# Kernel tuning notes

Hardware: AMD Instinct MI355X
Metric: run time of the kernel (lower is better)

## Reference

```python
import jax, jax.numpy as jnp
import numpy as np


def _flip_sequences(inputs, lengths):
    # Keeps padding at the end while reversing the valid prefix (per example).
    T = inputs.shape[1]
    def one(x, L):
        return jnp.flip(jnp.roll(x, T - L, axis=0), axis=0)
    return jax.vmap(one)(inputs, lengths)


def _gru_direction(xy, mask, Wi, Wh, bi, bhn):
    # xy: [B,T,D], mask: [B,T] (True = padding -> carry old state)
    B = xy.shape[0]
    H = bhn.shape[0]
    h0 = jnp.zeros((B, H), xy.dtype)
    xs = jnp.moveaxis(xy, 1, 0)    # [T,B,D]
    ms = jnp.moveaxis(mask, 1, 0)  # [T,B]

    def step(h, inp):
        x_t, m_t = inp
        gi = x_t @ Wi + bi          # [B,3H] input projections (r,z,n)
        gh = h @ Wh                 # [B,3H] hidden projections
        gi_r, gi_z, gi_n = jnp.split(gi, 3, axis=-1)
        gh_r, gh_z, gh_n = jnp.split(gh, 3, axis=-1)
        r = jax.nn.sigmoid(gi_r + gh_r)
        z = jax.nn.sigmoid(gi_z + gh_z)
        n = jnp.tanh(gi_n + r * (gh_n + bhn))
        new_h = (1.0 - z) * n + z * h
        h_next = jnp.where(m_t[:, None], h, new_h)  # mask: keep old state on padding
        return h_next, new_h

    _, outs = jax.lax.scan(step, h0, (xs, ms))
    return jnp.moveaxis(outs, 0, 1)  # [B,T,H]


def setup_inputs() -> dict:
    key = jax.random.key(0)
    ks = jax.random.split(key, 12)
    B, T, N, E, H = 256, 1000, 128, 4, 256
    D = N + E
    s = 0.08
    return {
        "spike_inputs": jax.random.normal(ks[0], (B, T, N), jnp.float32),
        "external_inputs": jax.random.normal(ks[1], (B, T, E), jnp.float32),
        "trial_lengths": jax.random.randint(ks[2], (B,), 1, T + 1),
        "Wi_f": jax.random.normal(ks[3], (D, 3 * H), jnp.float32) * s,
        "Wh_f": jax.random.normal(ks[4], (H, 3 * H), jnp.float32) * s,
        "bi_f": jnp.zeros((3 * H,), jnp.float32),
        "bhn_f": jnp.zeros((H,), jnp.float32),
        "Wi_b": jax.random.normal(ks[5], (D, 3 * H), jnp.float32) * s,
        "Wh_b": jax.random.normal(ks[6], (H, 3 * H), jnp.float32) * s,
        "bi_b": jnp.zeros((3 * H,), jnp.float32),
        "bhn_b": jnp.zeros((H,), jnp.float32),
    }


def reference(spike_inputs, external_inputs, trial_lengths,
              Wi_f, Wh_f, bi_f, bhn_f, Wi_b, Wh_b, bi_b, bhn_b):
    B, T = spike_inputs.shape[:2]
    # mask_sequences: True where t >= trial length (padding)
    mask = jnp.arange(T)[None, :] >= trial_lengths[:, None]  # [B,T]

    # forward direction
    xy_f = jnp.concatenate([spike_inputs, external_inputs], axis=-1)
    fwd = _gru_direction(xy_f, mask, Wi_f, Wh_f, bi_f, bhn_f)

    # backward direction on flipped sequences (padding stays at the end,
    # so the padding mask is identical)
    rs = _flip_sequences(spike_inputs, trial_lengths)
    re = _flip_sequences(external_inputs, trial_lengths)
    xy_b = jnp.concatenate([rs, re], axis=-1)
    bwd = _gru_direction(xy_b, mask, Wi_b, Wh_b, bi_b, bhn_b)
    bwd = _flip_sequences(bwd, trial_lengths)

    return jnp.concatenate([fwd, bwd], axis=-1)  # [B,T,2H]
```

## Files before the change

### kernel.cpp

```cpp
#include <hip/hip_runtime.h>

#define T_SEQ 1000
#define NS 128
#define NE 4
#define DIN 132
#define G3 768
#define WGS 512
#define NWG 128

typedef __attribute__((ext_vector_type(8))) short short8;
typedef __attribute__((ext_vector_type(4))) float floatx4;

#define STAMP_OFF 0
#define HX_OFF    4096
#define HX_BYTES  (32*2*8192)
#define WS_ZERO_BYTES (HX_OFF + HX_BYTES)

#define MFMA16(a,b,c) __builtin_amdgcn_mfma_f32_16x16x32_bf16((a),(b),(c),0,0,0)

__device__ __forceinline__ unsigned short f2bf(float f){
  unsigned u = __float_as_uint(f);
  return (unsigned short)((u + 0x7FFFu + ((u>>16)&1u)) >> 16);
}
__device__ __forceinline__ float bf2f(unsigned short b){
  return __uint_as_float(((unsigned)b)<<16);
}
__device__ __forceinline__ unsigned long long ld64a(const void* p){
  return __hip_atomic_load((const unsigned long long*)p, __ATOMIC_RELAXED, __HIP_MEMORY_SCOPE_AGENT);
}
__device__ __forceinline__ unsigned ld32a(const void* p){
  return __hip_atomic_load((const unsigned*)p, __ATOMIC_RELAXED, __HIP_MEMORY_SCOPE_AGENT);
}
__device__ __forceinline__ void st32a(void* p, unsigned v){
  __hip_atomic_store((unsigned*)p, v, __ATOMIC_RELAXED, __HIP_MEMORY_SCOPE_AGENT);
}

__global__ __launch_bounds__(WGS)
__attribute__((amdgpu_waves_per_eu(2, 2)))
void bigru6(
  const float* __restrict__ spike, const float* __restrict__ extin,
  const int* __restrict__ lens,
  const float* __restrict__ WiF, const float* __restrict__ WhF,
  const float* __restrict__ biF, const float* __restrict__ bhF,
  const float* __restrict__ WiB, const float* __restrict__ WhB,
  const float* __restrict__ biB, const float* __restrict__ bhB,
  float* __restrict__ out, char* __restrict__ ws)
{
  const int tid = threadIdx.x;
  const int bid = blockIdx.x;
  const int g   = bid >> 2;
  const int s   = bid & 3;
  const int dir = g >> 4;
  const int b_base = (g & 15) << 4;
  const int w  = tid >> 6;
  const int l  = tid & 63;
  const int dg = w >> 1;
  const int ks = w & 1;
  const int col = l & 15;
  const int q   = l >> 4;
  const int jd  = s*64 + dg*16 + col;

  const float* Wi  = dir ? WiB : WiF;
  const float* Wh  = dir ? WhB : WhF;
  const float* bi  = dir ? biB : biF;
  const float* bhn = dir ? bhB : bhF;

  __shared__ __align__(16) char  ldsXb[2*5*64*16];
  __shared__ __align__(16) float ldsC[4][4][16][20];
  __shared__ int ldsL[16];

  unsigned* stg = (unsigned*)(ws + STAMP_OFF) + g*16;
  char*     hxg = ws + HX_OFF + (size_t)g*2*8192;

  if (tid < 16) ldsL[tid] = lens[b_base + tid];
  for (int i = tid; i < 2*320; i += WGS)
    *(floatx4*)(ldsXb + i*16) = floatx4{0.f,0.f,0.f,0.f};
  __syncthreads();

  const int q8 = q*8;
  short8 Bh[4][3][2];
  short8 Bx[3][3][2];
  #pragma unroll
  for (int hk=0; hk<4; ++hk){
    const int k0 = (ks*4+hk)*32 + q8;
    #pragma unroll
    for (int gt=0; gt<3; ++gt){
      const int c = gt*256 + jd;
      #pragma unroll
      for (int i=0;i<8;++i){
        float wv = Wh[(size_t)(k0+i)*G3 + c];
        unsigned short hb = f2bf(wv);
        Bh[hk][gt][0][i] = (short)hb;
        Bh[hk][gt][1][i] = (short)f2bf(wv - bf2f(hb));
      }
    }
  }
  #pragma unroll
  for (int xk=0; xk<3; ++xk){
    const bool xv = (ks==0) || (xk<2);
    const int kxg = (ks==0) ? xk : (3+xk);
    const int k0 = kxg*32 + q8;
    #pragma unroll
    for (int gt=0; gt<3; ++gt){
      const int c = gt*256 + jd;
      #pragma unroll
      for (int i=0;i<8;++i){
        float wv = (xv && (k0+i) < DIN) ? Wi[(size_t)(k0+i)*G3 + c] : 0.f;
        unsigned short hb = f2bf(wv);
        Bx[xk][gt][0][i] = (short)hb;
        Bx[xk][gt][1][i] = (short)f2bf(wv - bf2f(hb));
      }
    }
  }

  const float bir = bi[jd], biz = bi[256+jd], bin = bi[512+jd], bhv = bhn[jd];
  int   Lr[4];
  float hold[4];
  #pragma unroll
  for (int j=0;j<4;++j){ Lr[j] = ldsL[q*4+j]; hold[j] = 0.f; }

  auto xload = [&](int m, int tt)->float4{
    const int row = m/33, pk = m - row*33, k0 = pk*4;
    const int L = ldsL[row];
    int tp = dir ? (L-1-tt) : tt;
    if (tp < 0) tp += T_SEQ;
    const size_t xb = (size_t)(b_base+row)*T_SEQ + tp;
    if (k0 < NS) return *(const float4*)(spike + xb*NS + k0);
    return *(const float4*)(extin + xb*NE);
  };
  auto xstore = [&](int m, float4 v, int buf){
    const int row = m/33, pk = m - row*33, k0 = pk*4;
    const int kg = k0>>5, sub = (k0>>3)&3, ii = k0&7;
    const int off = buf*5120 + ((kg*64 + row + 16*sub)*8 + ii)*2;
    unsigned lo = (unsigned)f2bf(v.x) | (((unsigned)f2bf(v.y))<<16);
    unsigned hi = (unsigned)f2bf(v.z) | (((unsigned)f2bf(v.w))<<16);
    *(unsigned*)(ldsXb + off)     = lo;
    *(unsigned*)(ldsXb + off + 4) = hi;
  };

  {
    float4 a = xload(tid, 0);  xstore(tid, a, 0);
    if (tid < 16){ float4 b = xload(tid+512, 0); xstore(tid+512, b, 0); }
  }
  __syncthreads();

  const int r0 = dg*64 + l;
  const int kg_o = jd >> 5, d5 = jd & 31;
  const int wslot = s*4 + dg;

  for (int t=0; t<T_SEQ; ++t){
    const int cur = t & 1, nxt = cur ^ 1;

    floatx4 aR={0.f,0.f,0.f,0.f}, aZ={0.f,0.f,0.f,0.f}, aNH={0.f,0.f,0.f,0.f}, aNX={0.f,0.f,0.f,0.f};
    if (ks==0){
      #pragma unroll
      for (int xk=0; xk<3; ++xk){
        const short8 a = *(const short8*)(ldsXb + (cur*320 + xk*64 + l)*16);
        aR  = MFMA16(a, Bx[xk][0][0], aR ); aZ  = MFMA16(a, Bx[xk][1][0], aZ ); aNX = MFMA16(a, Bx[xk][2][0], aNX);
        aR  = MFMA16(a, Bx[xk][0][1], aR ); aZ  = MFMA16(a, Bx[xk][1][1], aZ ); aNX = MFMA16(a, Bx[xk][2][1], aNX);
      }
    } else {
      #pragma unroll
      for (int xk=0; xk<2; ++xk){
        const short8 a = *(const short8*)(ldsXb + (cur*320 + (3+xk)*64 + l)*16);
        aR  = MFMA16(a, Bx[xk][0][0], aR ); aZ  = MFMA16(a, Bx[xk][1][0], aZ ); aNX = MFMA16(a, Bx[xk][2][0], aNX);
        aR  = MFMA16(a, Bx[xk][0][1], aR ); aZ  = MFMA16(a, Bx[xk][1][1], aZ ); aNX = MFMA16(a, Bx[xk][2][1], aNX);
      }
    }

    if (t > 0){
      const unsigned* sp = stg + (l & 15);
      while (true){
        unsigned v = ld32a(sp);
        if (__ballot(v >= (unsigned)t) == ~0ull) break;
        __builtin_amdgcn_s_sleep(1);
      }
      asm volatile("" ::: "memory");
    }

    short8 hf[4];
    {
      const char* hsrc = hxg + nxt*8192;
      #pragma unroll
      for (int hk=0; hk<4; ++hk){
        const char* p = hsrc + (((ks*4+hk)*64 + l)*16);
        union { unsigned long long qq[2]; short8 v; } u;
        u.qq[0] = ld64a(p); u.qq[1] = ld64a(p+8);
        hf[hk] = u.v;
      }
    }

    float4 sx0, sx1, sx2;
    if (ks==0 && t < T_SEQ-1){
      sx0 = xload(r0, t+1);
      sx1 = xload(r0+256, t+1);
      if (r0 < 16) sx2 = xload(r0+512, t+1);
    }

    #pragma unroll
    for (int hk=0; hk<4; ++hk){
      aR  = MFMA16(hf[hk], Bh[hk][0][0], aR ); aZ  = MFMA16(hf[hk], Bh[hk][1][0], aZ ); aNH = MFMA16(hf[hk], Bh[hk][2][0], aNH);
      aR  = MFMA16(hf[hk], Bh[hk][0][1], aR ); aZ  = MFMA16(hf[hk], Bh[hk][1][1], aZ ); aNH = MFMA16(hf[hk], Bh[hk][2][1], aNH);
    }

    if (ks==0){
      *(floatx4*)&ldsC[dg][0][col][q*4] = aR;
      *(floatx4*)&ldsC[dg][1][col][q*4] = aZ;
      *(floatx4*)&ldsC[dg][2][col][q*4] = aNH;
      *(floatx4*)&ldsC[dg][3][col][q*4] = aNX;
    }
    __syncthreads();

    if (ks==1){
      aR  += *(const floatx4*)&ldsC[dg][0][col][q*4];
      aZ  += *(const floatx4*)&ldsC[dg][1][col][q*4];
      aNH += *(const floatx4*)&ldsC[dg][2][col][q*4];
      aNX += *(const floatx4*)&ldsC[dg][3][col][q*4];
      unsigned dwj[4];
      float hnv[4];
      #pragma unroll
      for (int j=0;j<4;++j){
        const float gr = aR[j] + bir;
        const float gz = aZ[j] + biz;
        const float r = __fdividef(1.f, 1.f + __expf(-gr));
        const float z = __fdividef(1.f, 1.f + __expf(-gz));
        float pn = aNX[j] + bin + r*(aNH[j] + bhv);
        pn = fminf(fmaxf(pn, -20.f), 20.f);
        const float e2 = __expf(-2.f*pn);
        const float n  = __fdividef(1.f - e2, 1.f + e2);
        const float hn  = (1.f - z)*n + z*hold[j];
        const float hnx = (t < Lr[j]) ? hn : hold[j];
        hold[j] = hnx;
        hnv[j] = hn;
        unsigned bf = f2bf(hnx);
        unsigned ot = (unsigned)__shfl_xor((int)bf, 1);
        dwj[j] = (l & 1) ? 0u : (bf | (ot << 16));
      }
      if (t < T_SEQ-1){
        if ((l & 1) == 0){
          char* dst = hxg + cur*8192 + ((kg_o*64 + 16*(d5>>3))*16 + (d5&7)*2);
          #pragma unroll
          for (int j=0;j<4;++j)
            st32a(dst + (q*4+j)*16, dwj[j]);
        }
        asm volatile("s_waitcnt vmcnt(0)" ::: "memory");
        __builtin_amdgcn_sched_barrier(0);
        if (l == 0)
          st32a(stg + wslot, (unsigned)(t+1));
      }
      #pragma unroll
      for (int j=0;j<4;++j){
        const int rj = q*4 + j;
        int tp = dir ? (Lr[j]-1-t) : t;
        if (tp < 0) tp += T_SEQ;
        out[((size_t)(b_base+rj)*T_SEQ + tp)*512 + dir*256 + jd] = hnv[j];
      }
    } else {
      if (t < T_SEQ-1){
        xstore(r0, sx0, nxt);
        xstore(r0+256, sx1, nxt);
        if (r0 < 16) xstore(r0+512, sx2, nxt);
      }
    }
    __syncthreads();
  }
}

extern "C" void kernel_launch(void* const* d_in, const int* in_sizes, int n_in,
                              void* d_out, int out_size, void* d_ws, size_t ws_size,
                              hipStream_t stream) {
  (void)in_sizes; (void)n_in; (void)out_size; (void)ws_size;
  const float* spike = (const float*)d_in[0];
  const float* extin = (const float*)d_in[1];
  const int*   lens  = (const int*)  d_in[2];
  const float* WiF   = (const float*)d_in[3];
  const float* WhF   = (const float*)d_in[4];
  const float* biF   = (const float*)d_in[5];
  const float* bhF   = (const float*)d_in[6];
  const float* WiB   = (const float*)d_in[7];
  const float* WhB   = (const float*)d_in[8];
  const float* biB   = (const float*)d_in[9];
  const float* bhB   = (const float*)d_in[10];
  float* out = (float*)d_out;
  char* ws = (char*)d_ws;

  hipMemsetAsync(ws, 0, WS_ZERO_BYTES, stream);
  bigru6<<<dim3(NWG), dim3(WGS), 0, stream>>>(
      spike, extin, lens, WiF, WhF, biF, bhF, WiB, WhB, biB, bhB, out, ws);
}
```

Before: 4.811 ms.

## Interleave forward and backward GRU directions in one workgroup to overlap syncs

Each workgroup now handles both directions for the same batch group, halving the grid to 64 workgroups. Within a timestep it alternates forward and backward work, so the cross-workgroup wait for one direction's hidden state is hidden behind the other direction's MFMA work. Hidden state is staged through LDS after a single-wave poll that publishes an LDS flag, instead of every wave polling global memory. The cost is double the register weights per thread (the waves_per_eu hint is removed) and more serial work per workgroup.

```diff
diff --git a/kernel.cpp b/kernel.cpp
--- a/kernel.cpp
+++ b/kernel.cpp
@@ -6,7 +6,7 @@
 #define DIN 132
 #define G3 768
 #define WGS 512
-#define NWG 128
+#define NWG 64
 
 typedef __attribute__((ext_vector_type(8))) short short8;
 typedef __attribute__((ext_vector_type(4))) float floatx4;
@@ -34,10 +34,15 @@
 __device__ __forceinline__ void st32a(void* p, unsigned v){
   __hip_atomic_store((unsigned*)p, v, __ATOMIC_RELAXED, __HIP_MEMORY_SCOPE_AGENT);
 }
+__device__ __forceinline__ void flag_st(int* p, int v){
+  __hip_atomic_store(p, v, __ATOMIC_RELAXED, __HIP_MEMORY_SCOPE_WORKGROUP);
+}
+__device__ __forceinline__ int flag_ld(const int* p){
+  return __hip_atomic_load(p, __ATOMIC_RELAXED, __HIP_MEMORY_SCOPE_WORKGROUP);
+}
 
 __global__ __launch_bounds__(WGS)
-__attribute__((amdgpu_waves_per_eu(2, 2)))
-void bigru6(
+void bigru9(
   const float* __restrict__ spike, const float* __restrict__ extin,
   const int* __restrict__ lens,
   const float* __restrict__ WiF, const float* __restrict__ WhF,
@@ -48,10 +53,10 @@
 {
   const int tid = threadIdx.x;
   const int bid = blockIdx.x;
-  const int g   = bid >> 2;
+  const int gA  = bid >> 2;
+  const int gB  = gA + 16;
   const int s   = bid & 3;
-  const int dir = g >> 4;
-  const int b_base = (g & 15) << 4;
+  const int b_base = gA << 4;
   const int w  = tid >> 6;
   const int l  = tid & 63;
   const int dg = w >> 1;
@@ -60,26 +65,26 @@
   const int q   = l >> 4;
   const int jd  = s*64 + dg*16 + col;
 
-  const float* Wi  = dir ? WiB : WiF;
-  const float* Wh  = dir ? WhB : WhF;
-  const float* bi  = dir ? biB : biF;
-  const float* bhn = dir ? bhB : bhF;
-
-  __shared__ __align__(16) char  ldsXb[2*5*64*16];
-  __shared__ __align__(16) float ldsC[4][4][16][20];
+  __shared__ __align__(16) char  ldsXb[4*5*64*16];
+  __shared__ __align__(16) char  ldsA[8*64*16];
+  __shared__ __align__(16) float ldsC[2][4][4][16][20];
   __shared__ int ldsL[16];
-
-  unsigned* stg = (unsigned*)(ws + STAMP_OFF) + g*16;
-  char*     hxg = ws + HX_OFF + (size_t)g*2*8192;
+  __shared__ int flagA, flagB;
+
+  unsigned* stgA = (unsigned*)(ws + STAMP_OFF) + gA*16;
+  unsigned* stgB = (unsigned*)(ws + STAMP_OFF) + gB*16;
+  char*     hxA  = ws + HX_OFF + (size_t)gA*2*8192;
+  char*     hxB  = ws + HX_OFF + (size_t)gB*2*8192;
 
   if (tid < 16) ldsL[tid] = lens[b_base + tid];
-  for (int i = tid; i < 2*320; i += WGS)
+  if (tid == 0){ flagA = 0; flagB = 0; }
+  for (int i = tid; i < 4*320; i += WGS)
     *(floatx4*)(ldsXb + i*16) = floatx4{0.f,0.f,0.f,0.f};
   __syncthreads();
 
   const int q8 = q*8;
-  short8 Bh[4][3][2];
-  short8 Bx[3][3][2];
+  short8 BhA[4][3][2], BxA[3][3][2];
+  short8 BhB[4][3][2], BxB[3][3][2];
   #pragma unroll
   for (int hk=0; hk<4; ++hk){
     const int k0 = (ks*4+hk)*32 + q8;
@@ -88,10 +93,14 @@
       const int c = gt*256 + jd;
       #pragma unroll
       for (int i=0;i<8;++i){
-        float wv = Wh[(size_t)(k0+i)*G3 + c];
-        unsigned short hb = f2bf(wv);
-        Bh[hk][gt][0][i] = (short)hb;
-        Bh[hk][gt][1][i] = (short)f2bf(wv - bf2f(hb));
+        float wa = WhF[(size_t)(k0+i)*G3 + c];
+        unsigned short ha = f2bf(wa);
+        BhA[hk][gt][0][i] = (short)ha;
+        BhA[hk][gt][1][i] = (short)f2bf(wa - bf2f(ha));
+        float wb = WhB[(size_t)(k0+i)*G3 + c];
+        unsigned short hb = f2bf(wb);
+        BhB[hk][gt][0][i] = (short)hb;
+        BhB[hk][gt][1][i] = (short)f2bf(wb - bf2f(hb));
       }
     }
   }
@@ -105,33 +114,38 @@
       const int c = gt*256 + jd;
       #pragma unroll
       for (int i=0;i<8;++i){
-        float wv = (xv && (k0+i) < DIN) ? Wi[(size_t)(k0+i)*G3 + c] : 0.f;
-        unsigned short hb = f2bf(wv);
-        Bx[xk][gt][0][i] = (short)hb;
-        Bx[xk][gt][1][i] = (short)f2bf(wv - bf2f(hb));
+        float wa = (xv && (k0+i) < DIN) ? WiF[(size_t)(k0+i)*G3 + c] : 0.f;
+        unsigned short ha = f2bf(wa);
+        BxA[xk][gt][0][i] = (short)ha;
+        BxA[xk][gt][1][i] = (short)f2bf(wa - bf2f(ha));
+        float wb = (xv && (k0+i) < DIN) ? WiB[(size_t)(k0+i)*G3 + c] : 0.f;
+        unsigned short hb = f2bf(wb);
+        BxB[xk][gt][0][i] = (short)hb;
+        BxB[xk][gt][1][i] = (short)f2bf(wb - bf2f(hb));
       }
     }
   }
 
-  const float bir = bi[jd], biz = bi[256+jd], bin = bi[512+jd], bhv = bhn[jd];
+  const float birA = biF[jd], bizA = biF[256+jd], binA = biF[512+jd], bhvA = bhF[jd];
+  const float birB = biB[jd], bizB = biB[256+jd], binB = biB[512+jd], bhvB = bhB[jd];
   int   Lr[4];
-  float hold[4];
+  float holdA[4], holdB[4];
   #pragma unroll
-  for (int j=0;j<4;++j){ Lr[j] = ldsL[q*4+j]; hold[j] = 0.f; }
-
-  auto xload = [&](int m, int tt)->float4{
+  for (int j=0;j<4;++j){ Lr[j] = ldsL[q*4+j]; holdA[j] = 0.f; holdB[j] = 0.f; }
+
+  auto xloadD = [&](int m, int tt, int dirf)->float4{
     const int row = m/33, pk = m - row*33, k0 = pk*4;
     const int L = ldsL[row];
-    int tp = dir ? (L-1-tt) : tt;
+    int tp = dirf ? (L-1-tt) : tt;
     if (tp < 0) tp += T_SEQ;
     const size_t xb = (size_t)(b_base+row)*T_SEQ + tp;
     if (k0 < NS) return *(const float4*)(spike + xb*NS + k0);
     return *(const float4*)(extin + xb*NE);
   };
-  auto xstore = [&](int m, float4 v, int buf){
+  auto xstoreD = [&](int m, float4 v, int buf, int dirf){
     const int row = m/33, pk = m - row*33, k0 = pk*4;
     const int kg = k0>>5, sub = (k0>>3)&3, ii = k0&7;
-    const int off = buf*5120 + ((kg*64 + row + 16*sub)*8 + ii)*2;
+    const int off = dirf*10240 + buf*5120 + ((kg*64 + row + 16*sub)*8 + ii)*2;
     unsigned lo = (unsigned)f2bf(v.x) | (((unsigned)f2bf(v.y))<<16);
     unsigned hi = (unsigned)f2bf(v.z) | (((unsigned)f2bf(v.w))<<16);
     *(unsigned*)(ldsXb + off)     = lo;
@@ -139,8 +153,12 @@
   };
 
   {
-    float4 a = xload(tid, 0);  xstore(tid, a, 0);
-    if (tid < 16){ float4 b = xload(tid+512, 0); xstore(tid+512, b, 0); }
+    float4 a = xloadD(tid, 0, 0);  xstoreD(tid, a, 0, 0);
+    float4 b = xloadD(tid, 0, 1);  xstoreD(tid, b, 0, 1);
+    if (tid < 16){
+      float4 a2 = xloadD(tid+512, 0, 0); xstoreD(tid+512, a2, 0, 0);
+      float4 b2 = xloadD(tid+512, 0, 1); xstoreD(tid+512, b2, 0, 1);
+    }
   }
   __syncthreads();
 
@@ -151,116 +169,207 @@
   for (int t=0; t<T_SEQ; ++t){
     const int cur = t & 1, nxt = cur ^ 1;
 
+    float4 sa0, sa1, sa2, sb0, sb1, sb2;
+    if (ks==0 && t < T_SEQ-1){
+      sa0 = xloadD(r0, t+1, 0);      sb0 = xloadD(r0, t+1, 1);
+      sa1 = xloadD(r0+256, t+1, 0);  sb1 = xloadD(r0+256, t+1, 1);
+      if (r0 < 16){ sa2 = xloadD(r0+512, t+1, 0); sb2 = xloadD(r0+512, t+1, 1); }
+    }
+
     floatx4 aR={0.f,0.f,0.f,0.f}, aZ={0.f,0.f,0.f,0.f}, aNH={0.f,0.f,0.f,0.f}, aNX={0.f,0.f,0.f,0.f};
     if (ks==0){
       #pragma unroll
       for (int xk=0; xk<3; ++xk){
         const short8 a = *(const short8*)(ldsXb + (cur*320 + xk*64 + l)*16);
-        aR  = MFMA16(a, Bx[xk][0][0], aR ); aZ  = MFMA16(a, Bx[xk][1][0], aZ ); aNX = MFMA16(a, Bx[xk][2][0], aNX);
-        aR  = MFMA16(a, Bx[xk][0][1], aR ); aZ  = MFMA16(a, Bx[xk][1][1], aZ ); aNX = MFMA16(a, Bx[xk][2][1], aNX);
+        aR  = MFMA16(a, BxA[xk][0][0], aR ); aZ  = MFMA16(a, BxA[xk][1][0], aZ ); aNX = MFMA16(a, BxA[xk][2][0], aNX);
+        aR  = MFMA16(a, BxA[xk][0][1], aR ); aZ  = MFMA16(a, BxA[xk][1][1], aZ ); aNX = MFMA16(a, BxA[xk][2][1], aNX);
       }
     } else {
       #pragma unroll
       for (int xk=0; xk<2; ++xk){
         const short8 a = *(const short8*)(ldsXb + (cur*320 + (3+xk)*64 + l)*16);
-        aR  = MFMA16(a, Bx[xk][0][0], aR ); aZ  = MFMA16(a, Bx[xk][1][0], aZ ); aNX = MFMA16(a, Bx[xk][2][0], aNX);
-        aR  = MFMA16(a, Bx[xk][0][1], aR ); aZ  = MFMA16(a, Bx[xk][1][1], aZ ); aNX = MFMA16(a, Bx[xk][2][1], aNX);
+        aR  = MFMA16(a, BxA[xk][0][0], aR ); aZ  = MFMA16(a, BxA[xk][1][0], aZ ); aNX = MFMA16(a, BxA[xk][2][0], aNX);
+        aR  = MFMA16(a, BxA[xk][0][1], aR ); aZ  = MFMA16(a, BxA[xk][1][1], aZ ); aNX = MFMA16(a, BxA[xk][2][1], aNX);
       }
     }
 
     if (t > 0){
-      const unsigned* sp = stg + (l & 15);
+      if (w == 0){
+        const unsigned* sp = stgA + (l & 15);
+        while (true){
+          unsigned v = ld32a(sp);
+          if (__ballot(v >= (unsigned)t) == ~0ull) break;
+          __builtin_amdgcn_s_sleep(1);
+        }
+        if (l == 0) flag_st(&flagA, t);
+      }
+      while (flag_ld(&flagA) < t) __builtin_amdgcn_s_sleep(1);
+      asm volatile("" ::: "memory");
+    }
+    {
+      const char* p = hxA + nxt*8192 + tid*16;
+      union { unsigned long long qq[2]; short8 v; } u;
+      u.qq[0] = ld64a(p); u.qq[1] = ld64a(p+8);
+      *(short8*)(ldsA + tid*16) = u.v;
+    }
+    __syncthreads();
+
+    #pragma unroll
+    for (int hk=0; hk<4; ++hk){
+      const short8 a = *(const short8*)(ldsA + (((ks*4+hk)*64) + l)*16);
+      aR  = MFMA16(a, BhA[hk][0][0], aR ); aZ  = MFMA16(a, BhA[hk][1][0], aZ ); aNH = MFMA16(a, BhA[hk][2][0], aNH);
+      aR  = MFMA16(a, BhA[hk][0][1], aR ); aZ  = MFMA16(a, BhA[hk][1][1], aZ ); aNH = MFMA16(a, BhA[hk][2][1], aNH);
+    }
+    if (ks==0){
+      *(floatx4*)&ldsC[0][dg][0][col][q*4] = aR;
+      *(floatx4*)&ldsC[0][dg][1][col][q*4] = aZ;
+      *(floatx4*)&ldsC[0][dg][2][col][q*4] = aNH;
+      *(floatx4*)&ldsC[0][dg][3][col][q*4] = aNX;
+    }
+    if (w == 2 && t > 0){
+      const unsigned* sp = stgB + (l & 15);
       while (true){
         unsigned v = ld32a(sp);
         if (__ballot(v >= (unsigned)t) == ~0ull) break;
         __builtin_amdgcn_s_sleep(1);
       }
-      asm volatile("" ::: "memory");
-    }
-
-    short8 hf[4];
-    {
-      const char* hsrc = hxg + nxt*8192;
-      #pragma unroll
-      for (int hk=0; hk<4; ++hk){
-        const char* p = hsrc + (((ks*4+hk)*64 + l)*16);
-        union { unsigned long long qq[2]; short8 v; } u;
-        u.qq[0] = ld64a(p); u.qq[1] = ld64a(p+8);
-        hf[hk] = u.v;
-      }
-    }
-
-    float4 sx0, sx1, sx2;
-    if (ks==0 && t < T_SEQ-1){
-      sx0 = xload(r0, t+1);
-      sx1 = xload(r0+256, t+1);
-      if (r0 < 16) sx2 = xload(r0+512, t+1);
-    }
-
-    #pragma unroll
-    for (int hk=0; hk<4; ++hk){
-      aR  = MFMA16(hf[hk], Bh[hk][0][0], aR ); aZ  = MFMA16(hf[hk], Bh[hk][1][0], aZ ); aNH = MFMA16(hf[hk], Bh[hk][2][0], aNH);
-      aR  = MFMA16(hf[hk], Bh[hk][0][1], aR ); aZ  = MFMA16(hf[hk], Bh[hk][1][1], aZ ); aNH = MFMA16(hf[hk], Bh[hk][2][1], aNH);
-    }
-
-    if (ks==0){
-      *(floatx4*)&ldsC[dg][0][col][q*4] = aR;
-      *(floatx4*)&ldsC[dg][1][col][q*4] = aZ;
-      *(floatx4*)&ldsC[dg][2][col][q*4] = aNH;
-      *(floatx4*)&ldsC[dg][3][col][q*4] = aNX;
-    }
-    __syncthreads();
-
+      if (l == 0) flag_st(&flagB, t);
+    }
+    __syncthreads();
+
+    float hnvA[4];
+    unsigned dwjA[4];
     if (ks==1){
-      aR  += *(const floatx4*)&ldsC[dg][0][col][q*4];
-      aZ  += *(const floatx4*)&ldsC[dg][1][col][q*4];
-      aNH += *(const floatx4*)&ldsC[dg][2][col][q*4];
-      aNX += *(const floatx4*)&ldsC[dg][3][col][q*4];
-      unsigned dwj[4];
-      float hnv[4];
+      aR  += *(const floatx4*)&ldsC[0][dg][0][col][q*4];
+      aZ  += *(const floatx4*)&ldsC[0][dg][1][col][q*4];
+      aNH += *(const floatx4*)&ldsC[0][dg][2][col][q*4];
+      aNX += *(const floatx4*)&ldsC[0][dg][3][col][q*4];
       #pragma unroll
       for (int j=0;j<4;++j){
-        const float gr = aR[j] + bir;
-        const float gz = aZ[j] + biz;
+        const float gr = aR[j] + birA;
+        const float gz = aZ[j] + bizA;
         const float r = __fdividef(1.f, 1.f + __expf(-gr));
         const float z = __fdividef(1.f, 1.f + __expf(-gz));
-        float pn = aNX[j] + bin + r*(aNH[j] + bhv);
+        float pn = aNX[j] + binA + r*(aNH[j] + bhvA);
         pn = fminf(fmaxf(pn, -20.f), 20.f);
         const float e2 = __expf(-2.f*pn);
         const float n  = __fdividef(1.f - e2, 1.f + e2);
-        const float hn  = (1.f - z)*n + z*hold[j];
-        const float hnx = (t < Lr[j]) ? hn : hold[j];
-        hold[j] = hnx;
-        hnv[j] = hn;
+        const float hn  = (1.f - z)*n + z*holdA[j];
+        const float hnx = (t < Lr[j]) ? hn : holdA[j];
+        holdA[j] = hnx;
+        hnvA[j] = hn;
         unsigned bf = f2bf(hnx);
         unsigned ot = (unsigned)__shfl_xor((int)bf, 1);
-        dwj[j] = (l & 1) ? 0u : (bf | (ot << 16));
+        dwjA[j] = (l & 1) ? 0u : (bf | (ot << 16));
+      }
+      if (t < T_SEQ-1 && (l & 1) == 0){
+        char* dst = hxA + cur*8192 + ((kg_o*64 + 16*(d5>>3))*16 + (d5&7)*2);
+        #pragma unroll
+        for (int j=0;j<4;++j)
+          st32a(dst + (q*4+j)*16, dwjA[j]);
+      }
+    } else if (t < T_SEQ-1){
+      xstoreD(r0, sa0, nxt, 0);
+      xstoreD(r0+256, sa1, nxt, 0);
+      if (r0 < 16) xstoreD(r0+512, sa2, nxt, 0);
+    }
+
+    floatx4 bR={0.f,0.f,0.f,0.f}, bZ={0.f,0.f,0.f,0.f}, bNH={0.f,0.f,0.f,0.f}, bNX={0.f,0.f,0.f,0.f};
+    if (ks==0){
+      #pragma unroll
+      for (int xk=0; xk<3; ++xk){
+        const short8 a = *(const short8*)(ldsXb + ((640 + cur*320) + xk*64 + l)*16);
+        bR  = MFMA16(a, BxB[xk][0][0], bR ); bZ  = MFMA16(a, BxB[xk][1][0], bZ ); bNX = MFMA16(a, BxB[xk][2][0], bNX);
+        bR  = MFMA16(a, BxB[xk][0][1], bR ); bZ  = MFMA16(a, BxB[xk][1][1], bZ ); bNX = MFMA16(a, BxB[xk][2][1], bNX);
+      }
+    } else {
+      #pragma unroll
+      for (int xk=0; xk<2; ++xk){
+        const short8 a = *(const short8*)(ldsXb + ((640 + cur*320) + (3+xk)*64 + l)*16);
+        bR  = MFMA16(a, BxB[xk][0][0], bR ); bZ  = MFMA16(a, BxB[xk][1][0], bZ ); bNX = MFMA16(a, BxB[xk][2][0], bNX);
+        bR  = MFMA16(a, BxB[xk][0][1], bR ); bZ  = MFMA16(a, BxB[xk][1][1], bZ ); bNX = MFMA16(a, BxB[xk][2][1], bNX);
+      }
+    }
+    if (ks==1 && t < T_SEQ-1){
+      asm volatile("s_waitcnt vmcnt(0)" ::: "memory");
+      __builtin_amdgcn_sched_barrier(0);
+      if (l == 0) st32a(stgA + wslot, (unsigned)(t+1));
+    }
+
+    if (t > 0){
+      while (flag_ld(&flagB) < t) __builtin_amdgcn_s_sleep(1);
+      asm volatile("" ::: "memory");
+    }
+    {
+      const char* p = hxB + nxt*8192 + tid*16;
+      union { unsigned long long qq[2]; short8 v; } u;
+      u.qq[0] = ld64a(p); u.qq[1] = ld64a(p+8);
+      *(short8*)(ldsA + tid*16) = u.v;
+    }
+    __syncthreads();
+
+    #pragma unroll
+    for (int hk=0; hk<4; ++hk){
+      const short8 a = *(const short8*)(ldsA + (((ks*4+hk)*64) + l)*16);
+      bR  = MFMA16(a, BhB[hk][0][0], bR ); bZ  = MFMA16(a, BhB[hk][1][0], bZ ); bNH = MFMA16(a, BhB[hk][2][0], bNH);
+      bR  = MFMA16(a, BhB[hk][0][1], bR ); bZ  = MFMA16(a, BhB[hk][1][1], bZ ); bNH = MFMA16(a, BhB[hk][2][1], bNH);
+    }
+    if (ks==0){
+      *(floatx4*)&ldsC[1][dg][0][col][q*4] = bR;
+      *(floatx4*)&ldsC[1][dg][1][col][q*4] = bZ;
+      *(floatx4*)&ldsC[1][dg][2][col][q*4] = bNH;
+      *(floatx4*)&ldsC[1][dg][3][col][q*4] = bNX;
+    }
+    __syncthreads();
+
+    if (ks==1){
+      bR  += *(const floatx4*)&ldsC[1][dg][0][col][q*4];
+      bZ  += *(const floatx4*)&ldsC[1][dg][1][col][q*4];
+      bNH += *(const floatx4*)&ldsC[1][dg][2][col][q*4];
+      bNX += *(const floatx4*)&ldsC[1][dg][3][col][q*4];
+      float hnvB[4];
+      unsigned dwjB[4];
+      #pragma unroll
+      for (int j=0;j<4;++j){
+        const float gr = bR[j] + birB;
+        const float gz = bZ[j] + bizB;
+        const float r = __fdividef(1.f, 1.f + __expf(-gr));
+        const float z = __fdividef(1.f, 1.f + __expf(-gz));
+        float pn = bNX[j] + binB + r*(bNH[j] + bhvB);
+        pn = fminf(fmaxf(pn, -20.f), 20.f);
+        const float e2 = __expf(-2.f*pn);
+        const float n  = __fdividef(1.f - e2, 1.f + e2);
+        const float hn  = (1.f - z)*n + z*holdB[j];
+        const float hnx = (t < Lr[j]) ? hn : holdB[j];
+        holdB[j] = hnx;
+        hnvB[j] = hn;
+        unsigned bf = f2bf(hnx);
+        unsigned ot = (unsigned)__shfl_xor((int)bf, 1);
+        dwjB[j] = (l & 1) ? 0u : (bf | (ot << 16));
+      }
+      if (t < T_SEQ-1 && (l & 1) == 0){
+        char* dst = hxB + cur*8192 + ((kg_o*64 + 16*(d5>>3))*16 + (d5&7)*2);
+        #pragma unroll
+        for (int j=0;j<4;++j)
+          st32a(dst + (q*4+j)*16, dwjB[j]);
+      }
+      #pragma unroll
+      for (int j=0;j<4;++j){
+        const int rj = q*4 + j;
+        out[((size_t)(b_base+rj)*T_SEQ + t)*512 + jd] = hnvA[j];
+        int tp = Lr[j]-1-t;
+        if (tp < 0) tp += T_SEQ;
+        out[((size_t)(b_base+rj)*T_SEQ + tp)*512 + 256 + jd] = hnvB[j];
       }
       if (t < T_SEQ-1){
-        if ((l & 1) == 0){
-          char* dst = hxg + cur*8192 + ((kg_o*64 + 16*(d5>>3))*16 + (d5&7)*2);
-          #pragma unroll
-          for (int j=0;j<4;++j)
-            st32a(dst + (q*4+j)*16, dwj[j]);
-        }
         asm volatile("s_waitcnt vmcnt(0)" ::: "memory");
         __builtin_amdgcn_sched_barrier(0);
-        if (l == 0)
-          st32a(stg + wslot, (unsigned)(t+1));
-      }
-      #pragma unroll
-      for (int j=0;j<4;++j){
-        const int rj = q*4 + j;
-        int tp = dir ? (Lr[j]-1-t) : t;
-        if (tp < 0) tp += T_SEQ;
-        out[((size_t)(b_base+rj)*T_SEQ + tp)*512 + dir*256 + jd] = hnv[j];
-      }
-    } else {
-      if (t < T_SEQ-1){
-        xstore(r0, sx0, nxt);
-        xstore(r0+256, sx1, nxt);
-        if (r0 < 16) xstore(r0+512, sx2, nxt);
-      }
+        if (l == 0) st32a(stgB + wslot, (unsigned)(t+1));
+      }
+    } else if (t < T_SEQ-1){
+      xstoreD(r0, sb0, nxt, 1);
+      xstoreD(r0+256, sb1, nxt, 1);
+      if (r0 < 16) xstoreD(r0+512, sb2, nxt, 1);
     }
     __syncthreads();
   }
@@ -285,6 +394,6 @@
   char* ws = (char*)d_ws;
 
   hipMemsetAsync(ws, 0, WS_ZERO_BYTES, stream);
-  bigru6<<<dim3(NWG), dim3(WGS), 0, stream>>>(
+  bigru9<<<dim3(NWG), dim3(WGS), 0, stream>>>(
       spike, extin, lens, WiF, WhF, biF, bhF, WiB, WhB, biB, bhB, out, ws);
 }
```

New measurement: 18.88 ms. 292% more time.

## Interleave two batch groups per workgroup to overlap cross-workgroup sync latency

Applied to the files above, without the earlier changes.

Each workgroup now processes two independent 16-row batch groups back to back within every timestep, so the grid shrinks to 64 workgroups. The register-resident weight fragments are reused for both groups. The intent is that while one group spins waiting on the other workgroups' hidden-state stamps, those workgroups are finishing the other group, which hides the inter-workgroup handoff latency. In exchange, each workgroup's serial work per step roughly doubles and fewer CUs are used. The waves_per_eu hint is also removed.

```diff
diff --git a/kernel.cpp b/kernel.cpp
--- a/kernel.cpp
+++ b/kernel.cpp
@@ -6,7 +6,7 @@
 #define DIN 132
 #define G3 768
 #define WGS 512
-#define NWG 128
+#define NWG 64
 
 typedef __attribute__((ext_vector_type(8))) short short8;
 typedef __attribute__((ext_vector_type(4))) float floatx4;
@@ -36,8 +36,7 @@
 }
 
 __global__ __launch_bounds__(WGS)
-__attribute__((amdgpu_waves_per_eu(2, 2)))
-void bigru6(
+void bigru10(
   const float* __restrict__ spike, const float* __restrict__ extin,
   const int* __restrict__ lens,
   const float* __restrict__ WiF, const float* __restrict__ WhF,
@@ -48,10 +47,13 @@
 {
   const int tid = threadIdx.x;
   const int bid = blockIdx.x;
-  const int g   = bid >> 2;
-  const int s   = bid & 3;
-  const int dir = g >> 4;
-  const int b_base = (g & 15) << 4;
+  const int p  = (bid >> 2) & 7;
+  const int d  = bid >> 5;
+  const int s  = bid & 3;
+  const int gA = d*16 + p;
+  const int gB = gA + 8;
+  const int b_baseA = p << 4;
+  const int b_baseB = (p + 8) << 4;
   const int w  = tid >> 6;
   const int l  = tid & 63;
   const int dg = w >> 1;
@@ -60,20 +62,23 @@
   const int q   = l >> 4;
   const int jd  = s*64 + dg*16 + col;
 
-  const float* Wi  = dir ? WiB : WiF;
-  const float* Wh  = dir ? WhB : WhF;
-  const float* bi  = dir ? biB : biF;
-  const float* bhn = dir ? bhB : bhF;
-
-  __shared__ __align__(16) char  ldsXb[2*5*64*16];
-  __shared__ __align__(16) float ldsC[4][4][16][20];
-  __shared__ int ldsL[16];
-
-  unsigned* stg = (unsigned*)(ws + STAMP_OFF) + g*16;
-  char*     hxg = ws + HX_OFF + (size_t)g*2*8192;
-
-  if (tid < 16) ldsL[tid] = lens[b_base + tid];
-  for (int i = tid; i < 2*320; i += WGS)
+  const float* Wi  = d ? WiB : WiF;
+  const float* Wh  = d ? WhB : WhF;
+  const float* bi  = d ? biB : biF;
+  const float* bhn = d ? bhB : bhF;
+
+  __shared__ __align__(16) char  ldsXb[2*2*5*64*16];
+  __shared__ __align__(16) float ldsC[2][4][4][16][20];
+  __shared__ int ldsL[32];
+
+  unsigned* stgA = (unsigned*)(ws + STAMP_OFF) + gA*16;
+  unsigned* stgB = (unsigned*)(ws + STAMP_OFF) + gB*16;
+  char*     hxA  = ws + HX_OFF + (size_t)gA*2*8192;
+  char*     hxB  = ws + HX_OFF + (size_t)gB*2*8192;
+
+  if (tid < 16)      ldsL[tid]    = lens[b_baseA + tid];
+  else if (tid < 32) ldsL[tid]    = lens[b_baseB + tid - 16];
+  for (int i = tid; i < 2*2*320; i += WGS)
     *(floatx4*)(ldsXb + i*16) = floatx4{0.f,0.f,0.f,0.f};
   __syncthreads();
 
@@ -114,24 +119,28 @@
   }
 
   const float bir = bi[jd], biz = bi[256+jd], bin = bi[512+jd], bhv = bhn[jd];
-  int   Lr[4];
-  float hold[4];
+  int   LrA[4], LrB[4];
+  float holdA[4], holdB[4];
   #pragma unroll
-  for (int j=0;j<4;++j){ Lr[j] = ldsL[q*4+j]; hold[j] = 0.f; }
-
-  auto xload = [&](int m, int tt)->float4{
+  for (int j=0;j<4;++j){
+    LrA[j] = ldsL[q*4+j]; LrB[j] = ldsL[16+q*4+j];
+    holdA[j] = 0.f; holdB[j] = 0.f;
+  }
+
+  auto xloadG = [&](int m, int tt, int grp)->float4{
     const int row = m/33, pk = m - row*33, k0 = pk*4;
-    const int L = ldsL[row];
-    int tp = dir ? (L-1-tt) : tt;
+    const int L = ldsL[grp*16 + row];
+    int tp = d ? (L-1-tt) : tt;
     if (tp < 0) tp += T_SEQ;
-    const size_t xb = (size_t)(b_base+row)*T_SEQ + tp;
+    const int bb = grp ? b_baseB : b_baseA;
+    const size_t xb = (size_t)(bb+row)*T_SEQ + tp;
     if (k0 < NS) return *(const float4*)(spike + xb*NS + k0);
     return *(const float4*)(extin + xb*NE);
   };
-  auto xstore = [&](int m, float4 v, int buf){
+  auto xstoreG = [&](int m, float4 v, int buf, int grp){
     const int row = m/33, pk = m - row*33, k0 = pk*4;
     const int kg = k0>>5, sub = (k0>>3)&3, ii = k0&7;
-    const int off = buf*5120 + ((kg*64 + row + 16*sub)*8 + ii)*2;
+    const int off = grp*10240 + buf*5120 + ((kg*64 + row + 16*sub)*8 + ii)*2;
     unsigned lo = (unsigned)f2bf(v.x) | (((unsigned)f2bf(v.y))<<16);
     unsigned hi = (unsigned)f2bf(v.z) | (((unsigned)f2bf(v.w))<<16);
     *(unsigned*)(ldsXb + off)     = lo;
@@ -139,8 +148,12 @@
   };
 
   {
-    float4 a = xload(tid, 0);  xstore(tid, a, 0);
-    if (tid < 16){ float4 b = xload(tid+512, 0); xstore(tid+512, b, 0); }
+    float4 a = xloadG(tid, 0, 0);  xstoreG(tid, a, 0, 0);
+    float4 b = xloadG(tid, 0, 1);  xstoreG(tid, b, 0, 1);
+    if (tid < 16){
+      float4 a2 = xloadG(tid+512, 0, 0); xstoreG(tid+512, a2, 0, 0);
+      float4 b2 = xloadG(tid+512, 0, 1); xstoreG(tid+512, b2, 0, 1);
+    }
   }
   __syncthreads();
 
@@ -151,25 +164,32 @@
   for (int t=0; t<T_SEQ; ++t){
     const int cur = t & 1, nxt = cur ^ 1;
 
+    float4 sa0, sa1, sa2;
+    if (ks==0 && t < T_SEQ-1){
+      sa0 = xloadG(r0, t+1, 0);
+      sa1 = xloadG(r0+256, t+1, 0);
+      if (r0 < 16) sa2 = xloadG(r0+512, t+1, 0);
+    }
+
     floatx4 aR={0.f,0.f,0.f,0.f}, aZ={0.f,0.f,0.f,0.f}, aNH={0.f,0.f,0.f,0.f}, aNX={0.f,0.f,0.f,0.f};
     if (ks==0){
       #pragma unroll
       for (int xk=0; xk<3; ++xk){
-        const short8 a = *(const short8*)(ldsXb + (cur*320 + xk*64 + l)*16);
+        const short8 a = *(const short8*)(ldsXb + ((cur*320) + xk*64 + l)*16);
         aR  = MFMA16(a, Bx[xk][0][0], aR ); aZ  = MFMA16(a, Bx[xk][1][0], aZ ); aNX = MFMA16(a, Bx[xk][2][0], aNX);
         aR  = MFMA16(a, Bx[xk][0][1], aR ); aZ  = MFMA16(a, Bx[xk][1][1], aZ ); aNX = MFMA16(a, Bx[xk][2][1], aNX);
       }
     } else {
       #pragma unroll
       for (int xk=0; xk<2; ++xk){
-        const short8 a = *(const short8*)(ldsXb + (cur*320 + (3+xk)*64 + l)*16);
+        const short8 a = *(const short8*)(ldsXb + ((cur*320) + (3+xk)*64 + l)*16);
         aR  = MFMA16(a, Bx[xk][0][0], aR ); aZ  = MFMA16(a, Bx[xk][1][0], aZ ); aNX = MFMA16(a, Bx[xk][2][0], aNX);
         aR  = MFMA16(a, Bx[xk][0][1], aR ); aZ  = MFMA16(a, Bx[xk][1][1], aZ ); aNX = MFMA16(a, Bx[xk][2][1], aNX);
       }
     }
 
     if (t > 0){
-      const unsigned* sp = stg + (l & 15);
+      const unsigned* sp = stgA + (l & 15);
       while (true){
         unsigned v = ld32a(sp);
         if (__ballot(v >= (unsigned)t) == ~0ull) break;
@@ -178,44 +198,37 @@
       asm volatile("" ::: "memory");
     }
 
-    short8 hf[4];
+    short8 hfA[4];
     {
-      const char* hsrc = hxg + nxt*8192;
+      const char* hsrc = hxA + nxt*8192;
       #pragma unroll
       for (int hk=0; hk<4; ++hk){
-        const char* p = hsrc + (((ks*4+hk)*64 + l)*16);
+        const char* pp = hsrc + (((ks*4+hk)*64 + l)*16);
         union { unsigned long long qq[2]; short8 v; } u;
-        u.qq[0] = ld64a(p); u.qq[1] = ld64a(p+8);
-        hf[hk] = u.v;
-      }
-    }
-
-    float4 sx0, sx1, sx2;
-    if (ks==0 && t < T_SEQ-1){
-      sx0 = xload(r0, t+1);
-      sx1 = xload(r0+256, t+1);
-      if (r0 < 16) sx2 = xload(r0+512, t+1);
+        u.qq[0] = ld64a(pp); u.qq[1] = ld64a(pp+8);
+        hfA[hk] = u.v;
+      }
     }
 
     #pragma unroll
     for (int hk=0; hk<4; ++hk){
-      aR  = MFMA16(hf[hk], Bh[hk][0][0], aR ); aZ  = MFMA16(hf[hk], Bh[hk][1][0], aZ ); aNH = MFMA16(hf[hk], Bh[hk][2][0], aNH);
-      aR  = MFMA16(hf[hk], Bh[hk][0][1], aR ); aZ  = MFMA16(hf[hk], Bh[hk][1][1], aZ ); aNH = MFMA16(hf[hk], Bh[hk][2][1], aNH);
+      aR  = MFMA16(hfA[hk], Bh[hk][0][0], aR ); aZ  = MFMA16(hfA[hk], Bh[hk][1][0], aZ ); aNH = MFMA16(hfA[hk], Bh[hk][2][0], aNH);
+      aR  = MFMA16(hfA[hk], Bh[hk][0][1], aR ); aZ  = MFMA16(hfA[hk], Bh[hk][1][1], aZ ); aNH = MFMA16(hfA[hk], Bh[hk][2][1], aNH);
     }
 
     if (ks==0){
-      *(floatx4*)&ldsC[dg][0][col][q*4] = aR;
-      *(floatx4*)&ldsC[dg][1][col][q*4] = aZ;
-      *(floatx4*)&ldsC[dg][2][col][q*4] = aNH;
-      *(floatx4*)&ldsC[dg][3][col][q*4] = aNX;
+      *(floatx4*)&ldsC[0][dg][0][col][q*4] = aR;
+      *(floatx4*)&ldsC[0][dg][1][col][q*4] = aZ;
+      *(floatx4*)&ldsC[0][dg][2][col][q*4] = aNH;
+      *(floatx4*)&ldsC[0][dg][3][col][q*4] = aNX;
     }
     __syncthreads();
 
     if (ks==1){
-      aR  += *(const floatx4*)&ldsC[dg][0][col][q*4];
-      aZ  += *(const floatx4*)&ldsC[dg][1][col][q*4];
-      aNH += *(const floatx4*)&ldsC[dg][2][col][q*4];
-      aNX += *(const floatx4*)&ldsC[dg][3][col][q*4];
+      aR  += *(const floatx4*)&ldsC[0][dg][0][col][q*4];
+      aZ  += *(const floatx4*)&ldsC[0][dg][1][col][q*4];
+      aNH += *(const floatx4*)&ldsC[0][dg][2][col][q*4];
+      aNX += *(const floatx4*)&ldsC[0][dg][3][col][q*4];
       unsigned dwj[4];
       float hnv[4];
       #pragma unroll
@@ -228,9 +241,9 @@
         pn = fminf(fmaxf(pn, -20.f), 20.f);
         const float e2 = __expf(-2.f*pn);
         const float n  = __fdividef(1.f - e2, 1.f + e2);
-        const float hn  = (1.f - z)*n + z*hold[j];
-        const float hnx = (t < Lr[j]) ? hn : hold[j];
-        hold[j] = hnx;
+        const float hn  = (1.f - z)*n + z*holdA[j];
+        const float hnx = (t < LrA[j]) ? hn : holdA[j];
+        holdA[j] = hnx;
         hnv[j] = hn;
         unsigned bf = f2bf(hnx);
         unsigned ot = (unsigned)__shfl_xor((int)bf, 1);
@@ -238,7 +251,7 @@
       }
       if (t < T_SEQ-1){
         if ((l & 1) == 0){
-          char* dst = hxg + cur*8192 + ((kg_o*64 + 16*(d5>>3))*16 + (d5&7)*2);
+          char* dst = hxA + cur*8192 + ((kg_o*64 + 16*(d5>>3))*16 + (d5&7)*2);
           #pragma unroll
           for (int j=0;j<4;++j)
             st32a(dst + (q*4+j)*16, dwj[j]);
@@ -246,23 +259,134 @@
         asm volatile("s_waitcnt vmcnt(0)" ::: "memory");
         __builtin_amdgcn_sched_barrier(0);
         if (l == 0)
-          st32a(stg + wslot, (unsigned)(t+1));
+          st32a(stgA + wslot, (unsigned)(t+1));
       }
       #pragma unroll
       for (int j=0;j<4;++j){
         const int rj = q*4 + j;
-        int tp = dir ? (Lr[j]-1-t) : t;
+        int tp = d ? (LrA[j]-1-t) : t;
         if (tp < 0) tp += T_SEQ;
-        out[((size_t)(b_base+rj)*T_SEQ + tp)*512 + dir*256 + jd] = hnv[j];
+        out[((size_t)(b_baseA+rj)*T_SEQ + tp)*512 + d*256 + jd] = hnv[j];
       }
     } else {
       if (t < T_SEQ-1){
-        xstore(r0, sx0, nxt);
-        xstore(r0+256, sx1, nxt);
-        if (r0 < 16) xstore(r0+512, sx2, nxt);
-      }
+        xstoreG(r0, sa0, nxt, 0);
+        xstoreG(r0+256, sa1, nxt, 0);
+        if (r0 < 16) xstoreG(r0+512, sa2, nxt, 0);
+      }
+    }
+
+    float4 sb0, sb1, sb2;
+    if (ks==0 && t < T_SEQ-1){
+      sb0 = xloadG(r0, t+1, 1);
+      sb1 = xloadG(r0+256, t+1, 1);
+      if (r0 < 16) sb2 = xloadG(r0+512, t+1, 1);
+    }
+
+    floatx4 bR={0.f,0.f,0.f,0.f}, bZ={0.f,0.f,0.f,0.f}, bNH={0.f,0.f,0.f,0.f}, bNX={0.f,0.f,0.f,0.f};
+    if (ks==0){
+      #pragma unroll
+      for (int xk=0; xk<3; ++xk){
+        const short8 a = *(const short8*)(ldsXb + ((640 + cur*320) + xk*64 + l)*16);
+        bR  = MFMA16(a, Bx[xk][0][0], bR ); bZ  = MFMA16(a, Bx[xk][1][0], bZ ); bNX = MFMA16(a, Bx[xk][2][0], bNX);
+        bR  = MFMA16(a, Bx[xk][0][1], bR ); bZ  = MFMA16(a, Bx[xk][1][1], bZ ); bNX = MFMA16(a, Bx[xk][2][1], bNX);
+      }
+    } else {
+      #pragma unroll
+      for (int xk=0; xk<2; ++xk){
+        const short8 a = *(const short8*)(ldsXb + ((640 + cur*320) + (3+xk)*64 + l)*16);
+        bR  = MFMA16(a, Bx[xk][0][0], bR ); bZ  = MFMA16(a, Bx[xk][1][0], bZ ); bNX = MFMA16(a, Bx[xk][2][0], bNX);
+        bR  = MFMA16(a, Bx[xk][0][1], bR ); bZ  = MFMA16(a, Bx[xk][1][1], bZ ); bNX = MFMA16(a, Bx[xk][2][1], bNX);
+      }
+    }
+
+    if (t > 0){
+      const unsigned* sp = stgB + (l & 15);
+      while (true){
+        unsigned v = ld32a(sp);
+        if (__ballot(v >= (unsigned)t) == ~0ull) break;
+        __builtin_amdgcn_s_sleep(1);
+      }
+      asm volatile("" ::: "memory");
+    }
+
+    short8 hfB[4];
+    {
+      const char* hsrc = hxB + nxt*8192;
+      #pragma unroll
+      for (int hk=0; hk<4; ++hk){
+        const char* pp = hsrc + (((ks*4+hk)*64 + l)*16);
+        union { unsigned long long qq[2]; short8 v; } u;
+        u.qq[0] = ld64a(pp); u.qq[1] = ld64a(pp+8);
+        hfB[hk] = u.v;
+      }
+    }
+
+    #pragma unroll
+    for (int hk=0; hk<4; ++hk){
+      bR  = MFMA16(hfB[hk], Bh[hk][0][0], bR ); bZ  = MFMA16(hfB[hk], Bh[hk][1][0], bZ ); bNH = MFMA16(hfB[hk], Bh[hk][2][0], bNH);
+      bR  = MFMA16(hfB[hk], Bh[hk][0][1], bR ); bZ  = MFMA16(hfB[hk], Bh[hk][1][1], bZ ); bNH = MFMA16(hfB[hk], Bh[hk][2][1], bNH);
+    }
+
+    if (ks==0){
+      *(floatx4*)&ldsC[1][dg][0][col][q*4] = bR;
+      *(floatx4*)&ldsC[1][dg][1][col][q*4] = bZ;
+      *(floatx4*)&ldsC[1][dg][2][col][q*4] = bNH;
+      *(floatx4*)&ldsC[1][dg][3][col][q*4] = bNX;
     }
     __syncthreads();
+
+    if (ks==1){
+      bR  += *(const floatx4*)&ldsC[1][dg][0][col][q*4];
+      bZ  += *(const floatx4*)&ldsC[1][dg][1][col][q*4];
+      bNH += *(const floatx4*)&ldsC[1][dg][2][col][q*4];
+      bNX += *(const floatx4*)&ldsC[1][dg][3][col][q*4];
+      unsigned dwj[4];
+      float hnv[4];
+      #pragma unroll
+      for (int j=0;j<4;++j){
+        const float gr = bR[j] + bir;
+        const float gz = bZ[j] + biz;
+        const float r = __fdividef(1.f, 1.f + __expf(-gr));
+        const float z = __fdividef(1.f, 1.f + __expf(-gz));
+        float pn = bNX[j] + bin + r*(bNH[j] + bhv);
+        pn = fminf(fmaxf(pn, -20.f), 20.f);
+        const float e2 = __expf(-2.f*pn);
+        const float n  = __fdividef(1.f - e2, 1.f + e2);
+        const float hn  = (1.f - z)*n + z*holdB[j];
+        const float hnx = (t < LrB[j]) ? hn : holdB[j];
+        holdB[j] = hnx;
+        hnv[j] = hn;
+        unsigned bf = f2bf(hnx);
+        unsigned ot = (unsigned)__shfl_xor((int)bf, 1);
+        dwj[j] = (l & 1) ? 0u : (bf | (ot << 16));
+      }
+      if (t < T_SEQ-1){
+        if ((l & 1) == 0){
+          char* dst = hxB + cur*8192 + ((kg_o*64 + 16*(d5>>3))*16 + (d5&7)*2);
+          #pragma unroll
+          for (int j=0;j<4;++j)
+            st32a(dst + (q*4+j)*16, dwj[j]);
+        }
+        asm volatile("s_waitcnt vmcnt(0)" ::: "memory");
+        __builtin_amdgcn_sched_barrier(0);
+        if (l == 0)
+          st32a(stgB + wslot, (unsigned)(t+1));
+      }
+      #pragma unroll
+      for (int j=0;j<4;++j){
+        const int rj = q*4 + j;
+        int tp = d ? (LrB[j]-1-t) : t;
+        if (tp < 0) tp += T_SEQ;
+        out[((size_t)(b_baseB+rj)*T_SEQ + tp)*512 + d*256 + jd] = hnv[j];
+      }
+    } else {
+      if (t < T_SEQ-1){
+        xstoreG(r0, sb0, nxt, 1);
+        xstoreG(r0+256, sb1, nxt, 1);
+        if (r0 < 16) xstoreG(r0+512, sb2, nxt, 1);
+      }
+    }
   }
 }
 
@@ -285,6 +409,6 @@
   char* ws = (char*)d_ws;
 
   hipMemsetAsync(ws, 0, WS_ZERO_BYTES, stream);
-  bigru6<<<dim3(NWG), dim3(WGS), 0, stream>>>(
+  bigru10<<<dim3(NWG), dim3(WGS), 0, stream>>>(
       spike, extin, lens, WiF, WhF, biF, bhF, WiB, WhB, biB, bhB, out, ws);
 }
```

Measured after the change: 8.066 ms. 67.7% more time.
